# Kernel tuning notes

Measured on AMD Instinct MI355X. Metric: run time of the kernel, lower is better.

Reference implementation:

```python
import jax, jax.numpy as jnp
import numpy as np

HIDDEN = 4096
NUM_HEADS = 32
HEAD_DIM = HIDDEN // NUM_HEADS  # 128
ROPE_THETA = 10000.0
MAX_POS = 2048


def _rope_tables():
    inv_freq = 1.0 / (ROPE_THETA ** (jnp.arange(0, HEAD_DIM, 2, dtype=jnp.float32) / HEAD_DIM))
    t = jnp.arange(MAX_POS, dtype=jnp.float32)
    freqs = jnp.einsum('i,j->ij', t, inv_freq)          # [MAX_POS, HEAD_DIM/2]
    emb = jnp.concatenate([freqs, freqs], axis=-1)      # [MAX_POS, HEAD_DIM]
    return jnp.cos(emb), jnp.sin(emb)


def _apply_rotary(x, cos, sin):
    # x: [b, s, h, d]; cos/sin: [b, s, 1, d]
    half = x.shape[-1] // 2
    x_rot = jnp.concatenate([-x[..., half:], x[..., :half]], axis=-1)
    return x * cos + x_rot * sin


def setup_inputs() -> dict:
    key = jax.random.key(0)
    k1, k2, k3, k4, k5 = jax.random.split(key, 5)
    B, S = 1, 2048
    scale = 1.0 / np.sqrt(HIDDEN)
    return {
        'hidden_states': jax.random.normal(k1, (B, S, HIDDEN), dtype=jnp.float32),
        'position_ids': jnp.arange(S, dtype=jnp.int64).reshape(1, S),
        'wqkv_w': jax.random.normal(k2, (3 * HIDDEN, HIDDEN), dtype=jnp.float32) * scale,
        'wqkv_b': jax.random.normal(k3, (3 * HIDDEN,), dtype=jnp.float32) * 0.01,
        'wo_w': jax.random.normal(k4, (HIDDEN, HIDDEN), dtype=jnp.float32) * scale,
        'wo_b': jax.random.normal(k5, (HIDDEN,), dtype=jnp.float32) * 0.01,
    }


def reference(hidden_states, position_ids, wqkv_w, wqkv_b, wo_w, wo_b):
    b, s, _ = hidden_states.shape
    qkv = hidden_states @ wqkv_w.T + wqkv_b                  # [b, s, 3*hidden]
    qkv = qkv.reshape(b, s, NUM_HEADS, 3, HEAD_DIM)          # (h g d) layout
    q, k, v = qkv[..., 0, :], qkv[..., 1, :], qkv[..., 2, :]  # [b, s, h, d]

    cos_tab, sin_tab = _rope_tables()
    cos = cos_tab[position_ids][:, :, None, :]               # [b_or_1, s, 1, d]
    sin = sin_tab[position_ids][:, :, None, :]
    q = _apply_rotary(q, cos, sin)
    k = _apply_rotary(k, cos, sin)

    scores = jnp.einsum('bqhd,bkhd->bhqk', q, k) / jnp.sqrt(jnp.float32(HEAD_DIM))
    causal = jnp.tril(jnp.ones((s, s), dtype=bool))
    scores = jnp.where(causal[None, None, :, :], scores, -jnp.inf)
    attn = jax.nn.softmax(scores, axis=-1)
    out = jnp.einsum('bhqk,bkhd->bqhd', attn, v).reshape(b, s, HIDDEN)
    return out @ wo_w.T + wo_b
```

## Files before the change

kernel.cpp:

```cpp
#include <hip/hip_runtime.h>
#include <hip/hip_bf16.h>

typedef short bf16x8 __attribute__((ext_vector_type(8)));
typedef float f32x4  __attribute__((ext_vector_type(4)));

typedef __attribute__((address_space(1))) const unsigned int gu32_t;
typedef __attribute__((address_space(3))) unsigned int lu32_t;

__device__ inline void gld16(const void* g, void* l) {
  __builtin_amdgcn_global_load_lds((gu32_t*)g, (lu32_t*)l, 16, 0, 0);
}

#define S_LEN 2048
#define HID   4096
#define NH    32
#define HD    128
#define QKV_N 12288


__global__ void cvt_bf16_kernel(const float* __restrict__ in,
                                __hip_bfloat16* __restrict__ out, long n) {
  long stride = (long)gridDim.x * blockDim.x;
  for (long i = (long)blockIdx.x * blockDim.x + threadIdx.x; i * 8 < n; i += stride) {
    long b = i * 8;
    float4 a0 = *(const float4*)(in + b);
    float4 a1 = *(const float4*)(in + b + 4);
    union { __hip_bfloat16 h[8]; bf16x8 v; } u;
    u.h[0] = __float2bfloat16(a0.x); u.h[1] = __float2bfloat16(a0.y);
    u.h[2] = __float2bfloat16(a0.z); u.h[3] = __float2bfloat16(a0.w);
    u.h[4] = __float2bfloat16(a1.x); u.h[5] = __float2bfloat16(a1.y);
    u.h[6] = __float2bfloat16(a1.z); u.h[7] = __float2bfloat16(a1.w);
    *(bf16x8*)(out + b) = u.v;
  }
}

template<int WRITE_BF16>
__global__ __launch_bounds__(256) void gemm_bt_kernel(
    const __hip_bfloat16* __restrict__ A,
    const __hip_bfloat16* __restrict__ B,
    const float* __restrict__ bias,
    void* __restrict__ Cout, int M, int N, int K)
{
  __shared__ __hip_bfloat16 lA[128 * 64];
  __shared__ __hip_bfloat16 lB[128 * 64];
  const int t = threadIdx.x;
  const int w = t >> 6, l = t & 63;
  const int lr = l & 15, lg = l >> 4;
  const int m0 = blockIdx.x * 128, n0 = blockIdx.y * 128;
  const int wm = (w >> 1) * 64, wn = (w & 1) * 64;

  f32x4 acc[4][4] = {};

  for (int k0 = 0; k0 < K; k0 += 64) {
    #pragma unroll
    for (int i = 0; i < 4; ++i) {
      int c = i * 256 + t;
      int row = c >> 3, s = c & 7;
      gld16(A + (long)(m0 + row) * K + k0 + (s ^ (row & 7)) * 8, &lA[c * 8]);
    }
    #pragma unroll
    for (int i = 0; i < 4; ++i) {
      int c = i * 256 + t;
      int row = c >> 3, s = c & 7;
      gld16(B + (long)(n0 + row) * K + k0 + (s ^ (row & 7)) * 8, &lB[c * 8]);
    }
    __syncthreads();
    #pragma unroll
    for (int ks = 0; ks < 2; ++ks) {
      bf16x8 af[4], bfr[4];
      #pragma unroll
      for (int mi = 0; mi < 4; ++mi) {
        int row = wm + mi * 16 + lr;
        af[mi] = *(const bf16x8*)&lA[row * 64 + ((ks * 4 + lg) ^ (row & 7)) * 8];
      }
      #pragma unroll
      for (int ni = 0; ni < 4; ++ni) {
        int row = wn + ni * 16 + lr;
        bfr[ni] = *(const bf16x8*)&lB[row * 64 + ((ks * 4 + lg) ^ (row & 7)) * 8];
      }
      #pragma unroll
      for (int mi = 0; mi < 4; ++mi)
        #pragma unroll
        for (int ni = 0; ni < 4; ++ni)
          acc[mi][ni] = __builtin_amdgcn_mfma_f32_16x16x32_bf16(af[mi], bfr[ni], acc[mi][ni], 0, 0, 0);
    }
    __syncthreads();
  }

  #pragma unroll
  for (int mi = 0; mi < 4; ++mi) {
    #pragma unroll
    for (int ni = 0; ni < 4; ++ni) {
      int col = n0 + wn + ni * 16 + lr;
      float bv = bias[col];
      #pragma unroll
      for (int r = 0; r < 4; ++r) {
        int row = m0 + wm + mi * 16 + lg * 4 + r;
        float v = acc[mi][ni][r] + bv;
        if (WRITE_BF16)
          ((__hip_bfloat16*)Cout)[(long)row * N + col] = __float2bfloat16(v);
        else
          ((float*)Cout)[(long)row * N + col] = v;
      }
    }
  }
}

__global__ void rope_table_kernel(const int* __restrict__ pos,
                                  float* __restrict__ ct, float* __restrict__ st) {
  int s = blockIdx.x, j = threadIdx.x;
  float p = (float)pos[s];
  float invf = exp2f(-0.20762050593046013f * (float)j);
  float a = p * invf;
  ct[s * 64 + j] = cosf(a);
  st[s * 64 + j] = sinf(a);
}

__global__ __launch_bounds__(256) void rope_rearrange_kernel(
    const __hip_bfloat16* __restrict__ qkv,
    const float* __restrict__ ct, const float* __restrict__ st,
    __hip_bfloat16* __restrict__ Qr, __hip_bfloat16* __restrict__ Kr,
    __hip_bfloat16* __restrict__ Vt)
{
  __shared__ __hip_bfloat16 lv[64][136];
  const int h = blockIdx.y, s0 = blockIdx.x * 64, t = threadIdx.x;
  #pragma unroll
  for (int i = 0; i < 16; ++i) {
    int idx = i * 256 + t;
    int si = idx >> 6, j = idx & 63;
    long base = (long)(s0 + si) * QKV_N + h * 384;
    float c  = ct[(s0 + si) * 64 + j];
    float sn = st[(s0 + si) * 64 + j];
    float q1 = __bfloat162float(qkv[base + j]);
    float q2 = __bfloat162float(qkv[base + 64 + j]);
    float k1 = __bfloat162float(qkv[base + 128 + j]);
    float k2 = __bfloat162float(qkv[base + 192 + j]);
    long ob = (long)h * (S_LEN * HD) + (long)(s0 + si) * HD;
    Qr[ob + j]      = __float2bfloat16(q1 * c - q2 * sn);
    Qr[ob + 64 + j] = __float2bfloat16(q2 * c + q1 * sn);
    Kr[ob + j]      = __float2bfloat16(k1 * c - k2 * sn);
    Kr[ob + 64 + j] = __float2bfloat16(k2 * c + k1 * sn);
    lv[si][j]      = qkv[base + 256 + j];
    lv[si][64 + j] = qkv[base + 320 + j];
  }
  __syncthreads();
  #pragma unroll
  for (int i = 0; i < 4; ++i) {
    int c = i * 256 + t;
    int d = c >> 3, s8 = (c & 7) * 8;
    union { __hip_bfloat16 h8[8]; bf16x8 v; } u;
    #pragma unroll
    for (int j2 = 0; j2 < 8; ++j2) u.h8[j2] = lv[s8 + j2][d];
    *(bf16x8*)(Vt + (long)h * (HD * S_LEN) + (long)d * S_LEN + s0 + s8) = u.v;
  }
}

__global__ __launch_bounds__(256) void flash_attn_kernel(
    const __hip_bfloat16* __restrict__ Qr, const __hip_bfloat16* __restrict__ Kr,
    const __hip_bfloat16* __restrict__ Vt, __hip_bfloat16* __restrict__ O)
{
  __shared__ __hip_bfloat16 lK[64 * 128];
  __shared__ __hip_bfloat16 lV[128 * 64];
  __shared__ __hip_bfloat16 lP[4][16 * 72];
  const int h = blockIdx.y, pair = blockIdx.x;
  const int t = threadIdx.x, w = t >> 6, l = t & 63;
  const int lr = l & 15, lg = l >> 4;
  const __hip_bfloat16* Qh = Qr + (long)h * (S_LEN * HD);
  const __hip_bfloat16* Kh = Kr + (long)h * (S_LEN * HD);
  const __hip_bfloat16* Vh = Vt + (long)h * (HD * S_LEN);
  const float sc = 0.08838834764831845f;

  for (int ph = 0; ph < 2; ++ph) {
    const int qt = ph ? (31 - pair) : pair;
    const int q0 = qt * 64;

    bf16x8 qf[4];
    #pragma unroll
    for (int ks = 0; ks < 4; ++ks)
      qf[ks] = *(const bf16x8*)(Qh + (long)(q0 + w * 16 + lr) * HD + ks * 32 + lg * 8);

    float m_r[4], l_r[4];
    f32x4 oacc[8] = {};
    #pragma unroll
    for (int r = 0; r < 4; ++r) { m_r[r] = -1e30f; l_r[r] = 0.f; }

    const int ktiles = qt + 1;
    for (int kt = 0; kt < ktiles; ++kt) {
      const int k0 = kt * 64;
      #pragma unroll
      for (int i = 0; i < 4; ++i) {
        int c = i * 256 + t;
        int row = c >> 4, s = c & 15;
        gld16(Kh + (long)(k0 + row) * HD + (s ^ (row & 15)) * 8, &lK[c * 8]);
      }
      #pragma unroll
      for (int i = 0; i < 4; ++i) {
        int c = i * 256 + t;
        int d = c >> 3, s = c & 7;
        gld16(Vh + (long)d * S_LEN + k0 + (s ^ (d & 7)) * 8, &lV[c * 8]);
      }
      __syncthreads();

      f32x4 s[4] = {};
      #pragma unroll
      for (int ks = 0; ks < 4; ++ks) {
        bf16x8 kf[4];
        #pragma unroll
        for (int nf = 0; nf < 4; ++nf) {
          int row = nf * 16 + lr;
          kf[nf] = *(const bf16x8*)&lK[row * 128 + ((ks * 4 + lg) ^ (row & 15)) * 8];
        }
        #pragma unroll
        for (int nf = 0; nf < 4; ++nf)
          s[nf] = __builtin_amdgcn_mfma_f32_16x16x32_bf16(qf[ks], kf[nf], s[nf], 0, 0, 0);
      }

      #pragma unroll
      for (int r = 0; r < 4; ++r) {
        int q = q0 + w * 16 + lg * 4 + r;
        float mx = -1e30f;
        #pragma unroll
        for (int nf = 0; nf < 4; ++nf) {
          int k = k0 + nf * 16 + lr;
          float v = s[nf][r] * sc;
          if (k > q) v = -1e30f;
          s[nf][r] = v;
          mx = fmaxf(mx, v);
        }
        #pragma unroll
        for (int mk = 1; mk < 16; mk <<= 1) mx = fmaxf(mx, __shfl_xor(mx, mk));
        float mo = m_r[r];
        float mn = fmaxf(mo, mx);
        m_r[r] = mn;
        float alpha = __expf(mo - mn);
        float rs = 0.f;
        #pragma unroll
        for (int nf = 0; nf < 4; ++nf) {
          float p = __expf(s[nf][r] - mn);
          s[nf][r] = p;
          rs += p;
        }
        #pragma unroll
        for (int mk = 1; mk < 16; mk <<= 1) rs += __shfl_xor(rs, mk);
        l_r[r] = l_r[r] * alpha + rs;
        #pragma unroll
        for (int df = 0; df < 8; ++df) oacc[df][r] *= alpha;
      }

      #pragma unroll
      for (int nf = 0; nf < 4; ++nf)
        #pragma unroll
        for (int r = 0; r < 4; ++r)
          lP[w][(lg * 4 + r) * 72 + nf * 16 + lr] = __float2bfloat16(s[nf][r]);
      asm volatile("s_waitcnt lgkmcnt(0)" ::: "memory");

      #pragma unroll
      for (int ks2 = 0; ks2 < 2; ++ks2) {
        bf16x8 pa = *(const bf16x8*)&lP[w][lr * 72 + ks2 * 32 + lg * 8];
        #pragma unroll
        for (int df = 0; df < 8; ++df) {
          int row = df * 16 + lr;
          bf16x8 vf = *(const bf16x8*)&lV[row * 64 + ((ks2 * 4 + lg) ^ (row & 7)) * 8];
          oacc[df] = __builtin_amdgcn_mfma_f32_16x16x32_bf16(pa, vf, oacc[df], 0, 0, 0);
        }
      }
      __syncthreads();
    }

    #pragma unroll
    for (int r = 0; r < 4; ++r) {
      float inv = 1.f / l_r[r];
      long q = q0 + w * 16 + lg * 4 + r;
      #pragma unroll
      for (int df = 0; df < 8; ++df)
        O[q * HID + h * HD + df * 16 + lr] = __float2bfloat16(oacc[df][r] * inv);
    }
    __syncthreads();
  }
}

extern "C" void kernel_launch(void* const* d_in, const int* in_sizes, int n_in,
                              void* d_out, int out_size, void* d_ws, size_t ws_size,
                              hipStream_t stream)
{
  (void)in_sizes; (void)n_in; (void)out_size;
  const float* hidden = (const float*)d_in[0];
  const int*   pos    = (const int*)d_in[1];
  const float* wqkv_w = (const float*)d_in[2];
  const float* wqkv_b = (const float*)d_in[3];
  const float* wo_w   = (const float*)d_in[4];
  const float* wo_b   = (const float*)d_in[5];
  float* out = (float*)d_out;

  char* ws = (char*)d_ws;
  if (ws_size < 167772160UL) return;
  __hip_bfloat16* hid_bf  = (__hip_bfloat16*)(ws + 0);
  __hip_bfloat16* wqkv_bf = (__hip_bfloat16*)(ws + 16777216);
  __hip_bfloat16* qr      = (__hip_bfloat16*)(ws + 0);
  __hip_bfloat16* kr      = (__hip_bfloat16*)(ws + 16777216);
  __hip_bfloat16* vt      = (__hip_bfloat16*)(ws + 33554432);
  __hip_bfloat16* obf     = (__hip_bfloat16*)(ws + 50331648);
  __hip_bfloat16* wo_bf   = (__hip_bfloat16*)(ws + 67108864);
  float*          cos_t   = (float*)(ws + 100663296);
  float*          sin_t   = (float*)(ws + 100663296 + 524288);
  __hip_bfloat16* qkv_bf  = (__hip_bfloat16*)(ws + 117440512);

  cvt_bf16_kernel<<<4096, 256, 0, stream>>>(hidden, hid_bf, 8388608L);
  cvt_bf16_kernel<<<8192, 256, 0, stream>>>(wqkv_w, wqkv_bf, 50331648L);
  gemm_bt_kernel<1><<<dim3(16, 96), 256, 0, stream>>>(hid_bf, wqkv_bf, wqkv_b, qkv_bf, 2048, 12288, 4096);
  cvt_bf16_kernel<<<8192, 256, 0, stream>>>(wo_w, wo_bf, 16777216L);
  rope_table_kernel<<<2048, 64, 0, stream>>>(pos, cos_t, sin_t);
  rope_rearrange_kernel<<<dim3(32, 32), 256, 0, stream>>>(qkv_bf, cos_t, sin_t, qr, kr, vt);
  flash_attn_kernel<<<dim3(16, 32), 256, 0, stream>>>(qr, kr, vt, obf);
  gemm_bt_kernel<0><<<dim3(16, 32), 256, 0, stream>>>(obf, wo_bf, wo_b, out, 2048, 4096, 4096);
}
```

Baseline: 491.2 us.

## Add 256x256-tile pipelined QKV GEMM with double-buffered swizzled LDS

Replaces the generic 128x128 GEMM used for the QKV projection with a specialised kernel. It uses 256x256 tiles and 512 threads, double-buffered LDS filled by direct global-to-LDS loads, and an XOR swizzle. Loads for later k-steps are interleaved between MFMA phases, with setprio and explicit vmcnt waits. The goal is more data reuse per tile and overlap of memory traffic with matrix math. The cost is 128KB of LDS per block, which limits occupancy, and 384 blocks, which leaves a partial last wave on the CUs.

```diff
diff --git a/kernel.cpp b/kernel.cpp
--- a/kernel.cpp
+++ b/kernel.cpp
@@ -16,7 +16,6 @@
 #define NH    32
 #define HD    128
 #define QKV_N 12288
-
 
 __global__ void cvt_bf16_kernel(const float* __restrict__ in,
                                 __hip_bfloat16* __restrict__ out, long n) {
@@ -31,6 +30,105 @@
     u.h[4] = __float2bfloat16(a1.x); u.h[5] = __float2bfloat16(a1.y);
     u.h[6] = __float2bfloat16(a1.z); u.h[7] = __float2bfloat16(a1.w);
     *(bf16x8*)(out + b) = u.v;
+  }
+}
+
+
+#define G256_STAGE_A(sbuf, h, kt) do { int kk_ = (kt) * 64;                         \
+    _Pragma("unroll") for (int j_ = 0; j_ < 2; ++j_) {                              \
+      int row_ = j_ * 128 + (h) * 64 + (t >> 3);                 \
+      int sl_ = t & 7;                                                              \
+      gld16(Ag + (long)(m0 + row_) * 4096 + kk_ + (sl_ ^ (row_ & 7)) * 8,           \
+            &lA[sbuf][row_ * 64 + sl_ * 8]); } } while (0)
+
+#define G256_STAGE_B(sbuf, h, kt) do { int kk_ = (kt) * 64;                         \
+    _Pragma("unroll") for (int j_ = 0; j_ < 2; ++j_) {                              \
+      int g_ = t >> 8;                                                    \
+      int r32_ = (t >> 3) & 31;                                                     \
+      int row_ = (j_ * 2 + g_) * 64 + (h) * 32 + r32_;                              \
+      int sl_ = t & 7;                                                              \
+      gld16(Bg + (long)(n0 + row_) * 4096 + kk_ + (sl_ ^ (row_ & 7)) * 8,           \
+            &lB[sbuf][row_ * 64 + sl_ * 8]); } } while (0)
+
+#define G256_PHASE(buf, mh, nh, STAGE_STMT, VM) do {                                \
+    bf16x8 pa_[4][2], pb_[2][2];                                                    \
+    _Pragma("unroll") for (int mi_ = 0; mi_ < 4; ++mi_)                             \
+      _Pragma("unroll") for (int ks_ = 0; ks_ < 2; ++ks_) {                         \
+        int row_ = wr * 128 + (mh) * 64 + mi_ * 16 + lr;                            \
+        pa_[mi_][ks_] = *(const bf16x8*)&lA[buf][row_ * 64 +                        \
+                         ((ks_ * 4 + lg) ^ (row_ & 7)) * 8]; }                      \
+    _Pragma("unroll") for (int ni_ = 0; ni_ < 2; ++ni_)                             \
+      _Pragma("unroll") for (int ks_ = 0; ks_ < 2; ++ks_) {                         \
+        int row_ = wc * 64 + (nh) * 32 + ni_ * 16 + lr;                             \
+        pb_[ni_][ks_] = *(const bf16x8*)&lB[buf][row_ * 64 +                        \
+                         ((ks_ * 4 + lg) ^ (row_ & 7)) * 8]; }                      \
+    STAGE_STMT;                                                                     \
+    __builtin_amdgcn_s_barrier();                                                   \
+    __builtin_amdgcn_s_setprio(1);                                                  \
+    _Pragma("unroll") for (int mi_ = 0; mi_ < 4; ++mi_)                             \
+      _Pragma("unroll") for (int ni_ = 0; ni_ < 2; ++ni_)                           \
+        _Pragma("unroll") for (int ks_ = 0; ks_ < 2; ++ks_)                         \
+          acc[(mh) * 4 + mi_][(nh) * 2 + ni_] =                                     \
+            __builtin_amdgcn_mfma_f32_16x16x32_bf16(pa_[mi_][ks_], pb_[ni_][ks_],   \
+                acc[(mh) * 4 + mi_][(nh) * 2 + ni_], 0, 0, 0);                      \
+    __builtin_amdgcn_s_setprio(0);                                                  \
+    if (VM) { asm volatile("s_waitcnt vmcnt(4)" ::: "memory"); }                    \
+    __builtin_amdgcn_s_barrier();                                                   \
+    __builtin_amdgcn_sched_barrier(0);                                              \
+  } while (0)
+
+__global__ __launch_bounds__(512, 2) void gemm256_qkv_kernel(
+    const __hip_bfloat16* __restrict__ Ag,
+    const __hip_bfloat16* __restrict__ Bg,
+    const float* __restrict__ bias,
+    __hip_bfloat16* __restrict__ Cout)
+{
+  __shared__ __hip_bfloat16 lA[2][256 * 64];
+  __shared__ __hip_bfloat16 lB[2][256 * 64];
+  const int t = threadIdx.x;
+  const int w = t >> 6, l = t & 63;
+  const int wr = w >> 2, wc = w & 3;
+  const int lr = l & 15, lg = l >> 4;
+  const int m0 = blockIdx.x * 256, n0 = blockIdx.y * 256;
+
+  f32x4 acc[8][4] = {};
+
+  G256_STAGE_A(0, 0, 0); G256_STAGE_B(0, 0, 0);
+  G256_STAGE_A(0, 1, 0); G256_STAGE_B(0, 1, 0);
+  G256_STAGE_A(1, 0, 1); G256_STAGE_B(1, 0, 1);
+  asm volatile("s_waitcnt vmcnt(4)" ::: "memory");
+  __builtin_amdgcn_s_barrier();
+  __builtin_amdgcn_sched_barrier(0);
+
+  for (int i = 0; i < 32; ++i) {
+    const int T1 = 2 * i + 1;
+    const int T2 = (2 * i + 2) & 63;
+    const int T3 = (2 * i + 3) & 63;
+    G256_PHASE(0, 0, 0, G256_STAGE_A(1, 1, T1), 0);
+    G256_PHASE(0, 0, 1, G256_STAGE_B(1, 1, T1), 0);
+    G256_PHASE(0, 1, 0, G256_STAGE_A(0, 0, T2), 0);
+    G256_PHASE(0, 1, 1, G256_STAGE_B(0, 0, T2), 1);
+    G256_PHASE(1, 0, 0, G256_STAGE_A(0, 1, T2), 0);
+    G256_PHASE(1, 0, 1, G256_STAGE_B(0, 1, T2), 0);
+    G256_PHASE(1, 1, 0, G256_STAGE_A(1, 0, T3), 0);
+    G256_PHASE(1, 1, 1, G256_STAGE_B(1, 0, T3), 1);
+  }
+
+  asm volatile("s_waitcnt vmcnt(0)" ::: "memory");
+  __builtin_amdgcn_s_barrier();
+
+  #pragma unroll
+  for (int mi = 0; mi < 8; ++mi) {
+    #pragma unroll
+    for (int ni = 0; ni < 4; ++ni) {
+      int col = n0 + wc * 64 + ni * 16 + lr;
+      float bv = bias[col];
+      #pragma unroll
+      for (int r = 0; r < 4; ++r) {
+        int row = m0 + wr * 128 + mi * 16 + lg * 4 + r;
+        Cout[(long)row * QKV_N + col] = __float2bfloat16(acc[mi][ni][r] + bv);
+      }
+    }
   }
 }
 
@@ -307,7 +405,7 @@
 
   cvt_bf16_kernel<<<4096, 256, 0, stream>>>(hidden, hid_bf, 8388608L);
   cvt_bf16_kernel<<<8192, 256, 0, stream>>>(wqkv_w, wqkv_bf, 50331648L);
-  gemm_bt_kernel<1><<<dim3(16, 96), 256, 0, stream>>>(hid_bf, wqkv_bf, wqkv_b, qkv_bf, 2048, 12288, 4096);
+  gemm256_qkv_kernel<<<dim3(8, 48), 512, 0, stream>>>(hid_bf, wqkv_bf, wqkv_b, qkv_bf);
   cvt_bf16_kernel<<<8192, 256, 0, stream>>>(wo_w, wo_bf, 16777216L);
   rope_table_kernel<<<2048, 64, 0, stream>>>(pos, cos_t, sin_t);
   rope_rearrange_kernel<<<dim3(32, 32), 256, 0, stream>>>(qkv_bf, cos_t, sin_t, qr, kr, vt);
```

Result: slower. 550.5 us (+12.1%).

## Double-buffer K/V tiles in flash attention to prefetch next tile

Applied to the files above, without the earlier changes.

Splits the K and V shared-memory tiles into two buffers. The async global-to-LDS loads for the next key tile are issued before the current tile's QK^T, softmax and PV compute, so memory latency can overlap with MFMA work instead of stalling at a barrier each iteration. In exchange, LDS use per block roughly doubles, which can cut the number of resident blocks per CU. The end-of-iteration barrier is relied on to make sure the prefetched data has landed.

```diff
diff --git a/kernel.cpp b/kernel.cpp
--- a/kernel.cpp
+++ b/kernel.cpp
@@ -16,7 +16,6 @@
 #define NH    32
 #define HD    128
 #define QKV_N 12288
-
 
 __global__ void cvt_bf16_kernel(const float* __restrict__ in,
                                 __hip_bfloat16* __restrict__ out, long n) {
@@ -155,12 +154,28 @@
   }
 }
 
+#define FA_STAGE(buf, k0_) do {                                              \
+    _Pragma("unroll")                                                        \
+    for (int i_ = 0; i_ < 4; ++i_) {               \
+      int c_ = i_ * 256 + t;                                                 \
+      int row_ = c_ >> 4, s_ = c_ & 15;                                      \
+      gld16(Kh + (long)((k0_) + row_) * HD + (s_ ^ (row_ & 15)) * 8,         \
+            &lK[buf][c_ * 8]);                                               \
+    }                                                                        \
+    _Pragma("unroll")                                                        \
+    for (int i_ = 0; i_ < 4; ++i_) {             \
+      int c_ = i_ * 256 + t;                                                 \
+      int d_ = c_ >> 3, s_ = c_ & 7;                                         \
+      gld16(Vh + (long)d_ * S_LEN + (k0_) + (s_ ^ (d_ & 7)) * 8,             \
+            &lV[buf][c_ * 8]);                                               \
+    } } while (0)
+
 __global__ __launch_bounds__(256) void flash_attn_kernel(
     const __hip_bfloat16* __restrict__ Qr, const __hip_bfloat16* __restrict__ Kr,
     const __hip_bfloat16* __restrict__ Vt, __hip_bfloat16* __restrict__ O)
 {
-  __shared__ __hip_bfloat16 lK[64 * 128];
-  __shared__ __hip_bfloat16 lV[128 * 64];
+  __shared__ __hip_bfloat16 lK[2][64 * 128];
+  __shared__ __hip_bfloat16 lV[2][128 * 64];
   __shared__ __hip_bfloat16 lP[4][16 * 72];
   const int h = blockIdx.y, pair = blockIdx.x;
   const int t = threadIdx.x, w = t >> 6, l = t & 63;
@@ -185,21 +200,13 @@
     for (int r = 0; r < 4; ++r) { m_r[r] = -1e30f; l_r[r] = 0.f; }
 
     const int ktiles = qt + 1;
+    int cur = 0;
+    FA_STAGE(0, 0);
+    __syncthreads();
+
     for (int kt = 0; kt < ktiles; ++kt) {
       const int k0 = kt * 64;
-      #pragma unroll
-      for (int i = 0; i < 4; ++i) {
-        int c = i * 256 + t;
-        int row = c >> 4, s = c & 15;
-        gld16(Kh + (long)(k0 + row) * HD + (s ^ (row & 15)) * 8, &lK[c * 8]);
-      }
-      #pragma unroll
-      for (int i = 0; i < 4; ++i) {
-        int c = i * 256 + t;
-        int d = c >> 3, s = c & 7;
-        gld16(Vh + (long)d * S_LEN + k0 + (s ^ (d & 7)) * 8, &lV[c * 8]);
-      }
-      __syncthreads();
+      if (kt + 1 < ktiles) FA_STAGE(cur ^ 1, k0 + 64);
 
       f32x4 s[4] = {};
       #pragma unroll
@@ -208,7 +215,7 @@
         #pragma unroll
         for (int nf = 0; nf < 4; ++nf) {
           int row = nf * 16 + lr;
-          kf[nf] = *(const bf16x8*)&lK[row * 128 + ((ks * 4 + lg) ^ (row & 15)) * 8];
+          kf[nf] = *(const bf16x8*)&lK[cur][row * 128 + ((ks * 4 + lg) ^ (row & 15)) * 8];
         }
         #pragma unroll
         for (int nf = 0; nf < 4; ++nf)
@@ -260,11 +267,12 @@
         #pragma unroll
         for (int df = 0; df < 8; ++df) {
           int row = df * 16 + lr;
-          bf16x8 vf = *(const bf16x8*)&lV[row * 64 + ((ks2 * 4 + lg) ^ (row & 7)) * 8];
+          bf16x8 vf = *(const bf16x8*)&lV[cur][row * 64 + ((ks2 * 4 + lg) ^ (row & 7)) * 8];
           oacc[df] = __builtin_amdgcn_mfma_f32_16x16x32_bf16(pa, vf, oacc[df], 0, 0, 0);
         }
       }
       __syncthreads();
+      cur ^= 1;
     }
 
     #pragma unroll
```

Measured after the change: 489.1 us. Within noise of the previous version (-0.4%).
